# Kernel optimization log

Hardware: AMD Instinct MI355X
Metric: run time of the kernel (lower is better)

Reference implementation:

```python
import jax, jax.numpy as jnp
import numpy as np

N = 100000   # nodes
E = 1600000  # edges
D = 128      # out_feats
V = 5000     # annotation_size
L = 3        # n_steps SAGE layers


def setup_inputs() -> dict:
    key = jax.random.key(0)
    k0, k1, k2, k3, k4 = jax.random.split(key, 5)
    annotation = jax.random.randint(k0, (N,), 0, V)
    src = jax.random.randint(k1, (E,), 0, N)
    dst = jax.random.randint(k2, (E,), 0, N)
    emb = jax.random.normal(k3, (V, D), dtype=jnp.float32) * 0.02
    Ws = jax.random.normal(k4, (L, D, D), dtype=jnp.float32) / np.sqrt(D).astype(np.float32)
    bs = jnp.zeros((L, D), dtype=jnp.float32)
    return {"annotation": annotation, "src": src, "dst": dst, "emb": emb, "Ws": Ws, "bs": bs}


def reference(annotation, src, dst, emb, Ws, bs):
    # tok_embedding == 2: embedding lookup of node token ids
    h = emb[annotation]                                              # [N, D]
    # in-degree per destination node (constant across layers)
    deg = jax.ops.segment_sum(jnp.ones_like(src, dtype=jnp.float32), dst, num_segments=N)
    inv = 1.0 / (deg + 1.0)                                          # [N]
    # DGL SAGEConv, aggregator_type='gcn', eval mode (feat_drop is identity):
    #   h_neigh = (h_self + sum_{u->v} h_u) / (in_deg + 1); rst = relu(h_neigh @ W + b)
    for l in range(L):
        agg = jax.ops.segment_sum(h[src], dst, num_segments=N)       # [N, D] gather-scatter
        h = jax.nn.relu(((h + agg) * inv[:, None]) @ Ws[l] + bs[l])
    # residual=False -> merged node features are just h ('_merge_on nodes h')
    return h
```

## Files before the change

### kernel.cpp

```cpp
#include <hip/hip_runtime.h>
#include <hip/hip_fp16.h>


#define D 128
#define PBLK 128
#define BSH 7

typedef float f32x4 __attribute__((ext_vector_type(4)));
typedef _Float16 f16x8 __attribute__((ext_vector_type(8)));

__global__ __launch_bounds__(256) void k_hist(
    const int* __restrict__ dst, int* __restrict__ hist,
    int E, int chunk, int nbk) {
    __shared__ int lh[1024];
    int j = blockIdx.x, tid = threadIdx.x;
    for (int i = tid; i < nbk; i += 256) lh[i] = 0;
    __syncthreads();
    int e0 = j * chunk, e1 = min(E, e0 + chunk);
    for (int e = e0 + tid; e < e1; e += 256)
        atomicAdd(&lh[dst[e] >> BSH], 1);
    __syncthreads();
    for (int i = tid; i < nbk; i += 256) hist[(size_t)j * nbk + i] = lh[i];
}

__global__ void k_scan_offs(int* __restrict__ hist, int* __restrict__ tot, int nbk) {
    __shared__ int s[PBLK];
    int b = blockIdx.x, j = threadIdx.x;
    int v = hist[(size_t)j * nbk + b];
    s[j] = v;
    __syncthreads();
    for (int off = 1; off < PBLK; off <<= 1) {
        int x = (j >= off) ? s[j - off] : 0;
        __syncthreads();
        s[j] += x;
        __syncthreads();
    }
    hist[(size_t)j * nbk + b] = s[j] - v;
    if (j == PBLK - 1) tot[b] = s[j];
}

__global__ void k_scan_tot(int* __restrict__ tot, int* __restrict__ row_ptr,
                           int nbk, int N, int E) {
    __shared__ int s[1024];
    int t = threadIdx.x;
    int v = (t < nbk) ? tot[t] : 0;
    s[t] = v;
    __syncthreads();
    for (int off = 1; off < 1024; off <<= 1) {
        int x = (t >= off) ? s[t - off] : 0;
        __syncthreads();
        s[t] += x;
        __syncthreads();
    }
    if (t < nbk) tot[t] = s[t] - v;
    if (t == 0) { tot[nbk] = E; row_ptr[N] = E; }
}

__global__ __launch_bounds__(256) void k_scatter(
    const int* __restrict__ src, const int* __restrict__ dst,
    const int* __restrict__ ann, const int* __restrict__ hist,
    const int* __restrict__ tot, int2* __restrict__ tmp,
    int E, int chunk, int nbk) {
    __shared__ int cur[1024];
    int j = blockIdx.x, tid = threadIdx.x;
    for (int i = tid; i < nbk; i += 256)
        cur[i] = tot[i] + hist[(size_t)j * nbk + i];
    __syncthreads();
    int e0 = j * chunk, e1 = min(E, e0 + chunk);
    for (int e = e0 + tid; e < e1; e += 256) {
        int d = dst[e], s = src[e];
        int p = atomicAdd(&cur[d >> BSH], 1);
        tmp[p] = make_int2(s, ((d & ((1 << BSH) - 1)) << 13) | ann[s]);
    }
}

__global__ __launch_bounds__(256) void k_place(
    const int2* __restrict__ tmp, const int* __restrict__ tot,
    int* __restrict__ row_ptr, int2* __restrict__ eal, int N) {
    __shared__ int cnt[1 << BSH], sc[1 << BSH];
    int b = blockIdx.x, tid = threadIdx.x;
    int base = tot[b], end = tot[b + 1];
    if (tid < (1 << BSH)) cnt[tid] = 0;
    __syncthreads();
    for (int i = base + tid; i < end; i += 256)
        atomicAdd(&cnt[((unsigned)tmp[i].y) >> 13], 1);
    __syncthreads();
    if (tid < (1 << BSH)) sc[tid] = cnt[tid];
    __syncthreads();
    for (int off = 1; off < (1 << BSH); off <<= 1) {
        int x = (tid < (1 << BSH) && tid >= off) ? sc[tid - off] : 0;
        __syncthreads();
        if (tid < (1 << BSH)) sc[tid] += x;
        __syncthreads();
    }
    if (tid < (1 << BSH)) {
        int excl = sc[tid] - cnt[tid];
        int d0 = (b << BSH) + tid;
        if (d0 < N) row_ptr[d0] = base + excl;
        cnt[tid] = excl;
    }
    __syncthreads();
    for (int i = base + tid; i < end; i += 256) {
        int2 w = tmp[i];
        int p = atomicAdd(&cnt[((unsigned)w.y) >> 13], 1);
        eal[base + p] = make_int2(w.x, w.y & 0x1FFF);
    }
}

union H16Chunk { float4 f4; __half2 h2[4]; __half h[8]; };

__global__ void k_h16(const float* __restrict__ x, __half* __restrict__ y, int n8) {
    int i = blockIdx.x * blockDim.x + threadIdx.x;
    if (i >= n8) return;
    const float4* p = (const float4*)x;
    float4 a = p[2 * i], b = p[2 * i + 1];
    H16Chunk u;
    u.h2[0] = __floats2half2_rn(a.x, a.y);
    u.h2[1] = __floats2half2_rn(a.z, a.w);
    u.h2[2] = __floats2half2_rn(b.x, b.y);
    u.h2[3] = __floats2half2_rn(b.z, b.w);
    *(float4*)&y[8 * i] = u.f4;
}

#define XT_LD 136
__global__ __launch_bounds__(256) void k_gemm_mfma(
    const __half* __restrict__ x16, const float* __restrict__ W,
    __half* __restrict__ g16, int n, int ntiles) {
    __shared__ __half Bf[8 * 4 * 64 * 8];
    __shared__ __half Xt[64 * XT_LD];
    int tid = threadIdx.x;
    int lane = tid & 63;
    int wv = tid >> 6;

    for (int idx = tid; idx < 8 * 4 * 64; idx += 256) {
        int l = idx & 63, ks = (idx >> 6) & 3, nt = idx >> 8;
        int kq = (l >> 4) * 8;
        int col = nt * 16 + (l & 15);
        H16Chunk u;
        #pragma unroll
        for (int j = 0; j < 8; j++)
            u.h[j] = __float2half(W[(ks * 32 + kq + j) * 128 + col]);
        *(float4*)&Bf[idx * 8] = u.f4;
    }
    __syncthreads();

    f16x8 breg[8][4];
    #pragma unroll
    for (int nt = 0; nt < 8; nt++)
        #pragma unroll
        for (int ks = 0; ks < 4; ks++)
            breg[nt][ks] = *(f16x8*)&Bf[((nt * 4 + ks) * 64 + lane) * 8];

    int srow = tid >> 2;
    int sc = (tid & 3) * 32;
    int m = lane & 15, quad = lane >> 4;

    for (int tile = blockIdx.x; tile < ntiles; tile += gridDim.x) {
        int row0 = tile * 64;
        __syncthreads();
        {
            int gr = row0 + srow;
            if (gr >= n) gr = n - 1;
            const float4* xp = (const float4*)&x16[(size_t)gr * 128 + sc];
            float4 v0 = xp[0], v1 = xp[1], v2 = xp[2], v3 = xp[3];
            float4* xd = (float4*)&Xt[srow * XT_LD + sc];
            xd[0] = v0; xd[1] = v1; xd[2] = v2; xd[3] = v3;
        }
        __syncthreads();

        f32x4 acc[8];
        #pragma unroll
        for (int nt = 0; nt < 8; nt++) acc[nt] = (f32x4){0.f, 0.f, 0.f, 0.f};
        #pragma unroll
        for (int ks = 0; ks < 4; ks++) {
            f16x8 a = *(f16x8*)&Xt[(wv * 16 + m) * XT_LD + ks * 32 + quad * 8];
            #pragma unroll
            for (int nt = 0; nt < 8; nt++)
                acc[nt] = __builtin_amdgcn_mfma_f32_16x16x32_f16(a, breg[nt][ks], acc[nt], 0, 0, 0);
        }
        __syncthreads();
        #pragma unroll
        for (int nt = 0; nt < 8; nt++)
            #pragma unroll
            for (int r = 0; r < 4; r++)
                Xt[(wv * 16 + quad * 4 + r) * XT_LD + nt * 16 + m] = __float2half(acc[nt][r]);
        __syncthreads();
        {
            int gr = row0 + srow;
            if (gr < n) {
                float4* gp = (float4*)&g16[(size_t)gr * 128 + sc];
                float4* xs = (float4*)&Xt[srow * XT_LD + sc];
                gp[0] = xs[0]; gp[1] = xs[1]; gp[2] = xs[2]; gp[3] = xs[3];
            }
        }
    }
}

template<bool SELY, bool OUT32>
__global__ __launch_bounds__(256) void k_agg(
    const float4* __restrict__ tab, const int* __restrict__ selfidx,
    const int* __restrict__ row_ptr, const int2* __restrict__ eal,
    const float4* __restrict__ bias4,
    __half* __restrict__ h16out, float* __restrict__ f32out, int n) {
    int v = blockIdx.x * 4 + (threadIdx.x >> 6);
    int lane = threadIdx.x & 63;
    int g = lane >> 4;
    int q = lane & 15;
    int beg = row_ptr[v], end = row_ptr[v + 1];
    int deg = end - beg;
    float acc[8] = {};

    #define ACCUM(raw) do { H16Chunk u; u.f4 = (raw);                          \
        float2 t0 = __half22float2(u.h2[0]); acc[0] += t0.x; acc[1] += t0.y;   \
        float2 t1 = __half22float2(u.h2[1]); acc[2] += t1.x; acc[3] += t1.y;   \
        float2 t2 = __half22float2(u.h2[2]); acc[4] += t2.x; acc[5] += t2.y;   \
        float2 t3 = __half22float2(u.h2[3]); acc[6] += t3.x; acc[7] += t3.y; } while (0)
    #define IDX(w) (SELY ? (w).y : (w).x)

    if (g == 0) {
        int sr = SELY ? selfidx[v] : v;
        ACCUM(tab[(size_t)sr * 16 + q]);
    }

    int quads = deg >> 2;
    int p = 0;
    for (; p + 4 <= quads; p += 4) {
        int eb = beg + 4 * p + g;
        int2 w0 = eal[eb + 0], w1 = eal[eb + 4], w2 = eal[eb + 8], w3 = eal[eb + 12];
        float4 r0 = tab[(size_t)IDX(w0) * 16 + q], r1 = tab[(size_t)IDX(w1) * 16 + q];
        float4 r2 = tab[(size_t)IDX(w2) * 16 + q], r3 = tab[(size_t)IDX(w3) * 16 + q];
        ACCUM(r0); ACCUM(r1); ACCUM(r2); ACCUM(r3);
    }
    for (; p < quads; p++) ACCUM(tab[(size_t)IDX(eal[beg + 4 * p + g]) * 16 + q]);
    int tail = deg & 3;
    if (g < tail) ACCUM(tab[(size_t)IDX(eal[beg + 4 * quads + g]) * 16 + q]);
    #undef ACCUM
    #undef IDX

    #pragma unroll
    for (int j = 0; j < 8; j++) {
        acc[j] += __shfl_down(acc[j], 16, 64);
        acc[j] += __shfl_down(acc[j], 32, 64);
    }
    if (g == 0) {
        float sc = 1.0f / (float)(deg + 1);
        float4 b0 = bias4[2 * q], b1 = bias4[2 * q + 1];
        float o[8];
        o[0] = fmaxf(acc[0] * sc + b0.x, 0.f);
        o[1] = fmaxf(acc[1] * sc + b0.y, 0.f);
        o[2] = fmaxf(acc[2] * sc + b0.z, 0.f);
        o[3] = fmaxf(acc[3] * sc + b0.w, 0.f);
        o[4] = fmaxf(acc[4] * sc + b1.x, 0.f);
        o[5] = fmaxf(acc[5] * sc + b1.y, 0.f);
        o[6] = fmaxf(acc[6] * sc + b1.z, 0.f);
        o[7] = fmaxf(acc[7] * sc + b1.w, 0.f);
        if (!OUT32) {
            H16Chunk u;
            u.h2[0] = __floats2half2_rn(o[0], o[1]);
            u.h2[1] = __floats2half2_rn(o[2], o[3]);
            u.h2[2] = __floats2half2_rn(o[4], o[5]);
            u.h2[3] = __floats2half2_rn(o[6], o[7]);
            *(float4*)&h16out[(size_t)v * 128 + q * 8] = u.f4;
        } else {
            f32x4 a = {o[0], o[1], o[2], o[3]};
            f32x4 b = {o[4], o[5], o[6], o[7]};
            __builtin_nontemporal_store(a, (f32x4*)&f32out[(size_t)v * 128 + q * 8]);
            __builtin_nontemporal_store(b, (f32x4*)&f32out[(size_t)v * 128 + q * 8 + 4]);
        }
    }
}

extern "C" void kernel_launch(void* const* d_in, const int* in_sizes, int n_in,
                              void* d_out, int out_size, void* d_ws, size_t ws_size,
                              hipStream_t stream) {
    const int*   ann = (const int*)d_in[0];
    const int*   src = (const int*)d_in[1];
    const int*   dst = (const int*)d_in[2];
    const float* emb = (const float*)d_in[3];
    const float* Ws  = (const float*)d_in[4];
    const float* bs  = (const float*)d_in[5];
    float* out = (float*)d_out;

    const int N = in_sizes[0];
    const int E = in_sizes[1];
    const int V = in_sizes[3] / D;
    const int NT64 = (N + 63) / 64;
    const int VT64 = (V + 63) / 64;
    const int NBK  = (N + (1 << BSH) - 1) >> BSH;
    const int CHK  = (E + PBLK - 1) / PBLK;

    int*  deg     = (int*)d_ws;
    int*  row_ptr = deg + N;
    int*  bsum    = row_ptr + ((N + 1 + 3) & ~3);
    int2* eal     = (int2*)(bsum + 512);
    __half* hA16  = (__half*)(eal + E);
    __half* gB16  = hA16 + (size_t)N * D;
    __half* embW16= gB16 + (size_t)N * D;
    __half* emb16 = embW16 + (size_t)V * D;
    int2* tmp  = (int2*)hA16;
    int*  hist = (int*)gB16;
    int*  tot  = hist + (size_t)PBLK * NBK;

    k_h16<<<(V * D / 8 + 255) / 256, 256, 0, stream>>>(emb, emb16, V * D / 8);
    k_gemm_mfma<<<VT64, 256, 0, stream>>>(emb16, Ws, embW16, V, VT64);

    k_hist<<<PBLK, 256, 0, stream>>>(dst, hist, E, CHK, NBK);
    k_scan_offs<<<NBK, PBLK, 0, stream>>>(hist, tot, NBK);
    k_scan_tot<<<1, 1024, 0, stream>>>(tot, row_ptr, NBK, N, E);
    k_scatter<<<PBLK, 256, 0, stream>>>(src, dst, ann, hist, tot, tmp, E, CHK, NBK);
    k_place<<<NBK, 256, 0, stream>>>(tmp, tot, row_ptr, eal, N);

    k_agg<true, false><<<N / 4, 256, 0, stream>>>(
        (const float4*)embW16, ann, row_ptr, eal, (const float4*)bs,
        hA16, nullptr, N);

    k_gemm_mfma<<<512, 256, 0, stream>>>(hA16, Ws + (size_t)D * D, gB16, N, NT64);
    k_agg<false, false><<<N / 4, 256, 0, stream>>>(
        (const float4*)gB16, nullptr, row_ptr, eal, (const float4*)(bs + D),
        hA16, nullptr, N);

    k_gemm_mfma<<<512, 256, 0, stream>>>(hA16, Ws + (size_t)2 * D * D, gB16, N, NT64);
    k_agg<false, true><<<N / 4, 256, 0, stream>>>(
        (const float4*)gB16, nullptr, row_ptr, eal, (const float4*)(bs + 2 * D),
        nullptr, out, N);
}
```

Measured before the change: 417.5 us.

## Fuse neighbor aggregation with next-layer MFMA GEMM in one kernel

Adds a k_agg_gemm kernel that aggregates 64 rows of neighbor features into shared memory, applies the scale, bias and ReLU, then multiplies the tile by the next layer's weight with MFMA and writes the projected fp16 features. It replaces the separate aggregation and GEMM launches for the first two layers, removing the global round-trip of the intermediate hidden features and two kernel launches. In exchange each block holds the weight in LDS and runs 512 threads with 16 lanes per row, which may reduce occupancy and gather parallelism compared with the one-wave-per-node aggregation.

```diff
diff --git a/kernel.cpp b/kernel.cpp
--- a/kernel.cpp
+++ b/kernel.cpp
@@ -194,6 +194,125 @@
             }
         }
     }
+}
+
+template<bool SELY>
+__global__ __launch_bounds__(512) void k_agg_gemm(
+    const float4* __restrict__ tab, const int* __restrict__ selfidx,
+    const int* __restrict__ row_ptr, const int2* __restrict__ eal,
+    const float4* __restrict__ bias4, const float* __restrict__ W,
+    __half* __restrict__ g16, int n, int ntiles) {
+    __shared__ __half Bf[8 * 4 * 64 * 8];
+    __shared__ __half Xt[64 * XT_LD];
+    int tid = threadIdx.x;
+    int lane = tid & 63;
+    int wv = tid >> 6;
+    int unit = tid >> 4;
+    int ul = tid & 15;
+
+    for (int idx = tid; idx < 8 * 4 * 64; idx += 512) {
+        int l = idx & 63, ks = (idx >> 6) & 3, nt = idx >> 8;
+        int kq = (l >> 4) * 8;
+        int col = nt * 16 + (l & 15);
+        H16Chunk u;
+        #pragma unroll
+        for (int j = 0; j < 8; j++)
+            u.h[j] = __float2half(W[(ks * 32 + kq + j) * 128 + col]);
+        *(float4*)&Bf[idx * 8] = u.f4;
+    }
+    __syncthreads();
+
+    int m = lane & 15, quad = lane >> 4;
+    int stripe = wv >> 1;
+    int ntb = (wv & 1) * 4;
+
+    #define ACCUMK(A, raw) do { H16Chunk u; u.f4 = (raw);                      \
+        float2 t0 = __half22float2(u.h2[0]); A[0] += t0.x; A[1] += t0.y;       \
+        float2 t1 = __half22float2(u.h2[1]); A[2] += t1.x; A[3] += t1.y;       \
+        float2 t2 = __half22float2(u.h2[2]); A[4] += t2.x; A[5] += t2.y;       \
+        float2 t3 = __half22float2(u.h2[3]); A[6] += t3.x; A[7] += t3.y; } while (0)
+    #define IDX(w) (SELY ? (w).y : (w).x)
+
+    for (int tile = blockIdx.x; tile < ntiles; tile += gridDim.x) {
+        int row0 = tile * 64;
+        float acc[2][8] = {};
+        int degk[2];
+        #pragma unroll
+        for (int k = 0; k < 2; k++) {
+            int r = unit * 2 + k;
+            int v = row0 + r;
+            int vv = (v < n) ? v : 0;
+            int beg = row_ptr[vv];
+            int end = (v < n) ? row_ptr[vv + 1] : beg;
+            degk[k] = end - beg;
+            int sr = SELY ? selfidx[vv] : vv;
+            ACCUMK(acc[k], tab[(size_t)sr * 16 + ul]);
+            int p = beg;
+            for (; p + 4 <= end; p += 4) {
+                int2 w0 = eal[p], w1 = eal[p + 1], w2 = eal[p + 2], w3 = eal[p + 3];
+                float4 r0 = tab[(size_t)IDX(w0) * 16 + ul];
+                float4 r1 = tab[(size_t)IDX(w1) * 16 + ul];
+                float4 r2 = tab[(size_t)IDX(w2) * 16 + ul];
+                float4 r3 = tab[(size_t)IDX(w3) * 16 + ul];
+                ACCUMK(acc[k], r0); ACCUMK(acc[k], r1);
+                ACCUMK(acc[k], r2); ACCUMK(acc[k], r3);
+            }
+            for (; p < end; p++) ACCUMK(acc[k], tab[(size_t)IDX(eal[p]) * 16 + ul]);
+        }
+        __syncthreads();
+        {
+            float4 b0 = bias4[2 * ul], b1 = bias4[2 * ul + 1];
+            #pragma unroll
+            for (int k = 0; k < 2; k++) {
+                int r = unit * 2 + k;
+                float sc = 1.0f / (float)(degk[k] + 1);
+                H16Chunk u;
+                u.h2[0] = __floats2half2_rn(fmaxf(acc[k][0] * sc + b0.x, 0.f),
+                                            fmaxf(acc[k][1] * sc + b0.y, 0.f));
+                u.h2[1] = __floats2half2_rn(fmaxf(acc[k][2] * sc + b0.z, 0.f),
+                                            fmaxf(acc[k][3] * sc + b0.w, 0.f));
+                u.h2[2] = __floats2half2_rn(fmaxf(acc[k][4] * sc + b1.x, 0.f),
+                                            fmaxf(acc[k][5] * sc + b1.y, 0.f));
+                u.h2[3] = __floats2half2_rn(fmaxf(acc[k][6] * sc + b1.z, 0.f),
+                                            fmaxf(acc[k][7] * sc + b1.w, 0.f));
+                *(float4*)&Xt[r * XT_LD + ul * 8] = u.f4;
+            }
+        }
+        __syncthreads();
+        f32x4 cacc[4];
+        #pragma unroll
+        for (int t = 0; t < 4; t++) cacc[t] = (f32x4){0.f, 0.f, 0.f, 0.f};
+        #pragma unroll
+        for (int ks = 0; ks < 4; ks++) {
+            f16x8 a = *(f16x8*)&Xt[(stripe * 16 + m) * XT_LD + ks * 32 + quad * 8];
+            #pragma unroll
+            for (int t = 0; t < 4; t++) {
+                f16x8 b = *(f16x8*)&Bf[(((ntb + t) * 4 + ks) * 64 + lane) * 8];
+                cacc[t] = __builtin_amdgcn_mfma_f32_16x16x32_f16(a, b, cacc[t], 0, 0, 0);
+            }
+        }
+        __syncthreads();
+        #pragma unroll
+        for (int t = 0; t < 4; t++)
+            #pragma unroll
+            for (int r4 = 0; r4 < 4; r4++)
+                Xt[(stripe * 16 + quad * 4 + r4) * XT_LD + (ntb + t) * 16 + m] =
+                    __float2half(cacc[t][r4]);
+        __syncthreads();
+        {
+            int srow = tid >> 3, c = tid & 7;
+            int gr = row0 + srow;
+            float4 v0 = *(float4*)&Xt[srow * XT_LD + c * 16];
+            float4 v1 = *(float4*)&Xt[srow * XT_LD + c * 16 + 8];
+            if (gr < n) {
+                float4* gp = (float4*)&g16[(size_t)gr * 128 + c * 16];
+                gp[0] = v0;
+                gp[1] = v1;
+            }
+        }
+    }
+    #undef ACCUMK
+    #undef IDX
 }
 
 template<bool SELY, bool OUT32>
@@ -310,17 +429,15 @@
     k_scatter<<<PBLK, 256, 0, stream>>>(src, dst, ann, hist, tot, tmp, E, CHK, NBK);
     k_place<<<NBK, 256, 0, stream>>>(tmp, tot, row_ptr, eal, N);
 
-    k_agg<true, false><<<N / 4, 256, 0, stream>>>(
+    k_agg_gemm<true><<<NT64, 512, 0, stream>>>(
         (const float4*)embW16, ann, row_ptr, eal, (const float4*)bs,
-        hA16, nullptr, N);
-
-    k_gemm_mfma<<<512, 256, 0, stream>>>(hA16, Ws + (size_t)D * D, gB16, N, NT64);
-    k_agg<false, false><<<N / 4, 256, 0, stream>>>(
+        Ws + (size_t)D * D, gB16, N, NT64);
+
+    k_agg_gemm<false><<<NT64, 512, 0, stream>>>(
         (const float4*)gB16, nullptr, row_ptr, eal, (const float4*)(bs + D),
-        hA16, nullptr, N);
-
-    k_gemm_mfma<<<512, 256, 0, stream>>>(hA16, Ws + (size_t)2 * D * D, gB16, N, NT64);
+        Ws + (size_t)2 * D * D, hA16, N, NT64);
+
     k_agg<false, true><<<N / 4, 256, 0, stream>>>(
-        (const float4*)gB16, nullptr, row_ptr, eal, (const float4*)(bs + 2 * D),
+        (const float4*)hA16, nullptr, row_ptr, eal, (const float4*)(bs + 2 * D),
         nullptr, out, N);
 }
```

Measured after the change: 394.4 us. 5.5% less time.
